# Performance work log

Measured on AMD Instinct MI355X. Metric: run time of the kernel, lower is better.

Reference implementation:

```python
import jax, jax.numpy as jnp
import numpy as np

B, T, D = 16, 2048, 256

def setup_inputs() -> dict:
    key = jax.random.key(0)
    k1, k2, k3 = jax.random.split(key, 3)
    q = jax.random.normal(k1, (B, T, D), dtype=jnp.float32)
    a = jax.random.normal(k2, (B, T, D), dtype=jnp.float32)
    # original uses 'uniform' init; scale ~ small
    U = jax.random.uniform(k3, (D, D), dtype=jnp.float32, minval=-0.05, maxval=0.05)
    return {"q": q, "a": a, "U": U}

def reference(q, a, U):
    # G[b,i,j] = tanh( (q[b,i,:] @ U) . a[b,j,:] )
    qU = jnp.einsum('btd,de->bte', q, U)                 # [B,Tq,D]
    G = jnp.tanh(jnp.einsum('btd,bsd->bts', qU, a))      # [B,Tq,Ta]
    g_q = jax.nn.softmax(jnp.max(G, axis=-1), axis=1)    # [B,Tq]
    g_a = jax.nn.softmax(jnp.max(G, axis=1), axis=1)     # [B,Ta]
    q_out = jnp.einsum('btd,bt->bd', q, g_q)             # [B,D]
    a_out = jnp.einsum('bsd,bs->bd', a, g_a)             # [B,D]
    return (q_out, a_out)
```

## Files before the change

kernel.cpp:

```cpp
#include <hip/hip_runtime.h>
#include <stdint.h>

typedef __attribute__((ext_vector_type(8))) short s8v;
typedef __attribute__((ext_vector_type(4))) float f4v;

__device__ __forceinline__ unsigned short f2bf(float f) {
  unsigned u = __float_as_uint(f);
  u = u + 0x7FFFu + ((u >> 16) & 1u);
  return (unsigned short)(u >> 16);
}
__device__ __forceinline__ unsigned encf(float f) {
  unsigned i = __float_as_uint(f);
  return (i & 0x80000000u) ? ~i : (i | 0x80000000u);
}
__device__ __forceinline__ float decf(unsigned u) {
  unsigned i = (u & 0x80000000u) ? (u & 0x7FFFFFFFu) : ~u;
  return __uint_as_float(i);
}
__device__ __forceinline__ void gload_lds16(const unsigned short* g, unsigned short* l) {
  __builtin_amdgcn_global_load_lds((const __attribute__((address_space(1))) void*)g,
                                   (__attribute__((address_space(3))) void*)l, 16, 0, 0);
}

__global__ void convert_kernel(const float4* __restrict__ q, const float4* __restrict__ a,
                               const float* __restrict__ U,
                               ushort4* __restrict__ qb, ushort4* __restrict__ ab,
                               unsigned short* __restrict__ Ut,
                               unsigned* __restrict__ rcmax, float* __restrict__ out) {
  const int bx = blockIdx.x;
  if (bx < 8192) {
    const int i = bx * 256 + threadIdx.x;
    float4 v = q[i];
    qb[i] = make_ushort4(f2bf(v.x), f2bf(v.y), f2bf(v.z), f2bf(v.w));
    float4 w = a[i];
    ab[i] = make_ushort4(f2bf(w.x), f2bf(w.y), f2bf(w.z), f2bf(w.w));
  } else if (bx < 8256) {
    const int idx = (bx - 8192) * 256 + threadIdx.x;
    const int n  = idx >> 6;
    const int k4 = (idx & 63) * 4;
    ushort4 o;
    o.x = f2bf(U[(k4 + 0) * 256 + n]);
    o.y = f2bf(U[(k4 + 1) * 256 + n]);
    o.z = f2bf(U[(k4 + 2) * 256 + n]);
    o.w = f2bf(U[(k4 + 3) * 256 + n]);
    *(ushort4*)&Ut[n * 256 + k4] = o;
  } else if (bx < 8320) {
    const int idx = (bx - 8256) * 256 + threadIdx.x;
    *(uint4*)&rcmax[idx * 4] = make_uint4(0u, 0u, 0u, 0u);
  } else {
    out[(bx - 8320) * 256 + threadIdx.x] = 0.f;
  }
}

__global__ __attribute__((amdgpu_flat_work_group_size(512, 512), amdgpu_waves_per_eu(2, 2)))
void fused_qu_smax(const unsigned short* __restrict__ qb,
                   const unsigned short* __restrict__ Ut,
                   const unsigned short* __restrict__ ab,
                   unsigned* __restrict__ rowmax,
                   unsigned* __restrict__ colmax) {
  extern __shared__ char smem[];
  unsigned short* qUs    = (unsigned short*)smem;
  unsigned short* Bs2    = (unsigned short*)(smem + 65536);
  unsigned*       colLds = (unsigned*)(smem + 131072);
  unsigned*       rowLds = (unsigned*)(smem + 139264);

  const int tid = threadIdx.x;
  const int b = blockIdx.x, tm = blockIdx.y;

  const int lane = tid & 63;
  const int m16  = lane & 15;
  const int quad = lane >> 4;
  const int wave = tid >> 6;
  const int wm   = wave >> 2;
  const int wn   = wave & 3;
  const int wr32 = (wave >> 1) * 32;
  const int wc64 = (wave & 1) * 64;
  const int srow = tid >> 3;
  const int scol = (((tid & 7) ^ (srow & 7))) * 8;

  #pragma unroll
  for (int i = 0; i < 4; ++i) colLds[i * 512 + tid] = 0u;
  if (tid < 128) rowLds[tid] = 0u;

  const unsigned short* Aq = qb + ((long)b * 2048 + tm * 128) * 256;
  {
    f4v acc[4][4] = {};

#define STAGE1(kt, dst) do {                                                   \
    const int k0_ = (kt) * 64;                                                 \
    _Pragma("unroll")                                                          \
    for (int i_ = 0; i_ < 2; ++i_)                                             \
      gload_lds16(Aq + (long)(i_ * 64 + srow) * 256 + k0_ + scol,              \
                  &(dst)[i_ * 4096 + tid * 8]);                                \
    _Pragma("unroll")                                                          \
    for (int i_ = 0; i_ < 4; ++i_)                                             \
      gload_lds16(Ut + (long)(i_ * 64 + srow) * 256 + k0_ + scol,              \
                  &(dst)[8192 + i_ * 4096 + tid * 8]);                         \
  } while (0)

#define COMPUTE1(buf) do {                                                     \
    _Pragma("unroll")                                                          \
    for (int kk_ = 0; kk_ < 2; ++kk_) {                                        \
      const int cs_ = ((kk_ * 4 + quad) ^ (m16 & 7)) * 8;                      \
      s8v af_[4], bf_[4];                                                      \
      _Pragma("unroll")                                                        \
      for (int i_ = 0; i_ < 4; ++i_)                                           \
        af_[i_] = *(const s8v*)&(buf)[(wm * 64 + i_ * 16 + m16) * 64 + cs_];   \
      _Pragma("unroll")                                                        \
      for (int j_ = 0; j_ < 4; ++j_)                                           \
        bf_[j_] = *(const s8v*)&(buf)[8192 + (wn * 64 + j_ * 16 + m16) * 64 + cs_]; \
      _Pragma("unroll")                                                        \
      for (int i_ = 0; i_ < 4; ++i_)                                           \
        _Pragma("unroll")                                                      \
        for (int j_ = 0; j_ < 4; ++j_)                                         \
          acc[i_][j_] = __builtin_amdgcn_mfma_f32_16x16x32_bf16(af_[i_], bf_[j_], acc[i_][j_], 0, 0, 0); \
    }                                                                          \
  } while (0)

    STAGE1(0, Bs2);
    STAGE1(1, qUs);
    asm volatile("s_waitcnt vmcnt(6)" ::: "memory");
    __builtin_amdgcn_s_barrier();
    COMPUTE1(Bs2);
    __builtin_amdgcn_s_barrier();
    STAGE1(2, Bs2);
    asm volatile("s_waitcnt vmcnt(6)" ::: "memory");
    __builtin_amdgcn_s_barrier();
    COMPUTE1(qUs);
    __builtin_amdgcn_s_barrier();
    STAGE1(3, qUs);
    asm volatile("s_waitcnt vmcnt(6)" ::: "memory");
    __builtin_amdgcn_s_barrier();
    COMPUTE1(Bs2);
    asm volatile("s_waitcnt vmcnt(0)" ::: "memory");
    __builtin_amdgcn_s_barrier();
    COMPUTE1(qUs);
    __syncthreads();

    #pragma unroll
    for (int i = 0; i < 4; ++i)
      #pragma unroll
      for (int r = 0; r < 4; ++r) {
        const int lr = wm * 64 + i * 16 + quad * 4 + r;
        #pragma unroll
        for (int j = 0; j < 4; ++j) {
          const int col = wn * 64 + j * 16 + m16;
          const int ch = (col >> 3) ^ (lr & 7);
          qUs[lr * 256 + ch * 8 + (col & 7)] = f2bf(acc[i][j][r]);
        }
      }
  }
  __syncthreads();

  const unsigned short* Ab_ = ab + (long)b * 2048 * 256;

#define STAGE_TILE(tb, dst) do {                                               \
    _Pragma("unroll")                                                          \
    for (int e_ = 0; e_ < 8; ++e_) {                                           \
      const int u_ = e_ * 512 + tid;                                           \
      const int row_ = u_ >> 5;                                                \
      const int chs_ = (u_ & 31) ^ (row_ & 7);                                 \
      gload_lds16(Ab_ + (long)((tb) * 128 + row_) * 256 + chs_ * 8,            \
                  &(dst)[u_ * 8]);                                             \
    }                                                                          \
  } while (0)

#define COMPUTE_TILE(tb, buf) do {                                             \
    f4v acc[2][4] = {};                                                        \
    _Pragma("unroll")                                                          \
    for (int kq_ = 0; kq_ < 8; ++kq_) {                                        \
      const int cs_ = ((kq_ * 4 + quad) ^ (m16 & 7)) * 8;                      \
      _Pragma("unroll")                                                        \
      for (int j_ = 0; j_ < 4; ++j_) {                                         \
        const s8v bv_ = *(const s8v*)&(buf)[(wc64 + j_ * 16 + m16) * 256 + cs_]; \
        acc[0][j_] = __builtin_amdgcn_mfma_f32_16x16x32_bf16(aq[0][kq_], bv_, acc[0][j_], 0, 0, 0); \
        acc[1][j_] = __builtin_amdgcn_mfma_f32_16x16x32_bf16(aq[1][kq_], bv_, acc[1][j_], 0, 0, 0); \
      }                                                                        \
    }                                                                          \
    _Pragma("unroll")                                                          \
    for (int i_ = 0; i_ < 2; ++i_)                                             \
      _Pragma("unroll")                                                        \
      for (int r_ = 0; r_ < 4; ++r_)                                           \
        rmx[i_][r_] = fmaxf(rmx[i_][r_],                                       \
          fmaxf(fmaxf(acc[i_][0][r_], acc[i_][1][r_]),                         \
                fmaxf(acc[i_][2][r_], acc[i_][3][r_])));                       \
    _Pragma("unroll")                                                          \
    for (int j_ = 0; j_ < 4; ++j_) {                                           \
      float v_ = fmaxf(fmaxf(acc[0][j_][0], acc[0][j_][1]),                    \
                       fmaxf(acc[0][j_][2], acc[0][j_][3]));                   \
      v_ = fmaxf(v_, fmaxf(fmaxf(acc[1][j_][0], acc[1][j_][1]),                \
                           fmaxf(acc[1][j_][2], acc[1][j_][3])));              \
      v_ = fmaxf(v_, __shfl_xor(v_, 16));                                      \
      v_ = fmaxf(v_, __shfl_xor(v_, 32));                                      \
      if (quad == 0)                                                           \
        atomicMax(&colLds[(tb) * 128 + wc64 + j_ * 16 + m16], encf(v_));       \
    }                                                                          \
  } while (0)

  STAGE_TILE(0, Bs2);

  s8v aq[2][8];
  #pragma unroll
  for (int kq = 0; kq < 8; ++kq) {
    const int cs = ((kq * 4 + quad) ^ (m16 & 7)) * 8;
    aq[0][kq] = *(const s8v*)&qUs[(wr32 + m16) * 256 + cs];
    aq[1][kq] = *(const s8v*)&qUs[(wr32 + 16 + m16) * 256 + cs];
  }
  asm volatile("s_waitcnt lgkmcnt(0)" ::: "memory");
  __builtin_amdgcn_s_barrier();

  float rmx[2][4];
  #pragma unroll
  for (int i = 0; i < 2; ++i)
    #pragma unroll
    for (int r = 0; r < 4; ++r) rmx[i][r] = -3.4e38f;

  #pragma unroll 1
  for (int t2 = 0; t2 < 8; ++t2) {
    const int te = t2 * 2;
    STAGE_TILE(te + 1, qUs);
    asm volatile("s_waitcnt vmcnt(8)" ::: "memory");
    __builtin_amdgcn_s_barrier();
    COMPUTE_TILE(te, Bs2);
    __builtin_amdgcn_s_barrier();
    if (te + 2 < 16) {
      STAGE_TILE(te + 2, Bs2);
      asm volatile("s_waitcnt vmcnt(8)" ::: "memory");
    } else {
      asm volatile("s_waitcnt vmcnt(0)" ::: "memory");
    }
    __builtin_amdgcn_s_barrier();
    COMPUTE_TILE(te + 1, qUs);
    __builtin_amdgcn_s_barrier();
  }

  #pragma unroll
  for (int i = 0; i < 2; ++i)
    #pragma unroll
    for (int r = 0; r < 4; ++r) {
      float v = rmx[i][r];
      #pragma unroll
      for (int d2 = 1; d2 < 16; d2 <<= 1) v = fmaxf(v, __shfl_xor(v, d2));
      if (m16 == 0) atomicMax(&rowLds[wr32 + i * 16 + quad * 4 + r], encf(v));
    }
  __syncthreads();
  if (tid < 128)
    rowmax[(long)b * 2048 + tm * 128 + tid] = rowLds[tid];
  #pragma unroll
  for (int i = 0; i < 4; ++i)
    atomicMax(&colmax[(long)b * 2048 + i * 512 + tid], colLds[i * 512 + tid]);
}

__global__ void wsum_kernel(const uint4* __restrict__ qb, const uint4* __restrict__ ab,
                            const unsigned* __restrict__ rowmax, const unsigned* __restrict__ colmax,
                            float* __restrict__ out) {
  const int tid = threadIdx.x;
  const int chunk = blockIdx.x;
  const int b = blockIdx.y;
  const int z = blockIdx.z;
  const unsigned* e = z ? colmax : rowmax;
  const uint4* src = z ? ab : qb;

  __shared__ float sm[4];
  __shared__ float ss[4];
  __shared__ float wLds[128];
  __shared__ float red[256 * 8];

  float x[8];
  float m = -3.4e38f;
  #pragma unroll
  for (int j = 0; j < 8; ++j) {
    x[j] = tanhf(decf(e[b * 2048 + j * 256 + tid]));
    m = fmaxf(m, x[j]);
  }
  #pragma unroll
  for (int d2 = 1; d2 < 64; d2 <<= 1) m = fmaxf(m, __shfl_xor(m, d2));
  if ((tid & 63) == 0) sm[tid >> 6] = m;
  __syncthreads();
  m = fmaxf(fmaxf(sm[0], sm[1]), fmaxf(sm[2], sm[3]));
  float s = 0.f;
  #pragma unroll
  for (int j = 0; j < 8; ++j) s += expf(x[j] - m);
  #pragma unroll
  for (int d2 = 1; d2 < 64; d2 <<= 1) s += __shfl_xor(s, d2);
  if ((tid & 63) == 0) ss[tid >> 6] = s;
  __syncthreads();
  const float inv = 1.f / (ss[0] + ss[1] + ss[2] + ss[3]);

  if (tid < 128) {
    float xv = tanhf(decf(e[b * 2048 + chunk * 128 + tid]));
    wLds[tid] = expf(xv - m) * inv;
  }
  __syncthreads();

  const int dg = tid & 31;
  const int rg = tid >> 5;
  float acc[8] = {};
  const long rowbase = (long)b * 2048 + chunk * 128;
  for (int t = rg; t < 128; t += 8) {
    const float wgt = wLds[t];
    uint4 v = src[(rowbase + t) * 32 + dg];
    acc[0] += wgt * __uint_as_float(v.x << 16);
    acc[1] += wgt * __uint_as_float(v.x & 0xFFFF0000u);
    acc[2] += wgt * __uint_as_float(v.y << 16);
    acc[3] += wgt * __uint_as_float(v.y & 0xFFFF0000u);
    acc[4] += wgt * __uint_as_float(v.z << 16);
    acc[5] += wgt * __uint_as_float(v.z & 0xFFFF0000u);
    acc[6] += wgt * __uint_as_float(v.w << 16);
    acc[7] += wgt * __uint_as_float(v.w & 0xFFFF0000u);
  }
  #pragma unroll
  for (int k = 0; k < 8; ++k) red[tid * 8 + k] = acc[k];
  __syncthreads();
  if (tid < 32) {
    #pragma unroll
    for (int k = 0; k < 8; ++k) {
      float v = 0.f;
      #pragma unroll
      for (int g = 0; g < 8; ++g) v += red[((g << 5) | tid) * 8 + k];
      atomicAdd(&out[z * 4096 + b * 256 + tid * 8 + k], v);
    }
  }
}

extern "C" void kernel_launch(void* const* d_in, const int* in_sizes, int n_in,
                              void* d_out, int out_size, void* d_ws, size_t ws_size,
                              hipStream_t stream) {
  const float* q = (const float*)d_in[0];
  const float* a = (const float*)d_in[1];
  const float* U = (const float*)d_in[2];
  float* out = (float*)d_out;

  char* w = (char*)d_ws;
  unsigned short* qb = (unsigned short*)w;
  unsigned short* ab = (unsigned short*)(w + (16ull << 20));
  unsigned short* Ut = (unsigned short*)(w + (32ull << 20));
  unsigned* rmax = (unsigned*)(w + (32ull << 20) + (128ull << 10));
  unsigned* cmax = rmax + 32768;

  constexpr int SMEM = 139776;
  hipFuncSetAttribute((const void*)fused_qu_smax,
                      hipFuncAttributeMaxDynamicSharedMemorySize, SMEM);

  convert_kernel<<<8352, 256, 0, stream>>>((const float4*)q, (const float4*)a, U,
                                           (ushort4*)qb, (ushort4*)ab, Ut, rmax, out);

  fused_qu_smax<<<dim3(16, 16), 512, SMEM, stream>>>(qb, Ut, ab, rmax, cmax);

  wsum_kernel<<<dim3(16, 16, 2), 256, 0, stream>>>((const uint4*)qb, (const uint4*)ab,
                                                   rmax, cmax, out);
}
```

Measured before the change: 157.4 us.

## Restructure a-tile loop into 4-buffer 64-row pipeline with prefetch during qU phase

Replaces the double-buffered 128-row a-tile loop with a four-slot ring of 64-row tiles, three tiles in flight, so global loads overlap more MFMA work. The first a tiles are issued during the tail of the qU GEMM phase, and a full __syncthreads is replaced by an lgkmcnt wait plus barrier. The smaller tiles halve the MFMA work per barrier and double the number of barriers and colmax atomics. The reused LDS regions depend on correct wait counts.

```diff
diff --git a/kernel.cpp b/kernel.cpp
--- a/kernel.cpp
+++ b/kernel.cpp
@@ -63,6 +63,7 @@
   unsigned short* Bs2    = (unsigned short*)(smem + 65536);
   unsigned*       colLds = (unsigned*)(smem + 131072);
   unsigned*       rowLds = (unsigned*)(smem + 139264);
+#define SBUF(k) ((unsigned short*)(smem + ((k) << 15)))
 
   const int tid = threadIdx.x;
   const int b = blockIdx.x, tm = blockIdx.y;
@@ -74,13 +75,26 @@
   const int wm   = wave >> 2;
   const int wn   = wave & 3;
   const int wr32 = (wave >> 1) * 32;
-  const int wc64 = (wave & 1) * 64;
+  const int wc32 = (wave & 1) * 32;
   const int srow = tid >> 3;
   const int scol = (((tid & 7) ^ (srow & 7))) * 8;
 
   #pragma unroll
   for (int i = 0; i < 4; ++i) colLds[i * 512 + tid] = 0u;
   if (tid < 128) rowLds[tid] = 0u;
+
+  const unsigned short* Ab_ = ab + (long)b * 2048 * 256;
+
+#define STG64(tb, dst) do {                                                    \
+    _Pragma("unroll")                                                          \
+    for (int e_ = 0; e_ < 4; ++e_) {                                           \
+      const int u_ = e_ * 512 + tid;         \
+      const int row_ = u_ >> 5;                                                \
+      const int chs_ = (u_ & 31) ^ (row_ & 7);                                 \
+      gload_lds16(Ab_ + (long)((tb) * 64 + row_) * 256 + chs_ * 8,             \
+                  &(dst)[u_ * 8]);                                             \
+    }                                                                          \
+  } while (0)
 
   const unsigned short* Aq = qb + ((long)b * 2048 + tm * 128) * 256;
   {
@@ -134,8 +148,11 @@
     COMPUTE1(Bs2);
     asm volatile("s_waitcnt vmcnt(0)" ::: "memory");
     __builtin_amdgcn_s_barrier();
+    STG64(0, SBUF(2));
+    STG64(1, SBUF(3));
     COMPUTE1(qUs);
-    __syncthreads();
+    asm volatile("s_waitcnt lgkmcnt(0)" ::: "memory");
+    __builtin_amdgcn_s_barrier();
 
     #pragma unroll
     for (int i = 0; i < 4; ++i)
@@ -150,29 +167,34 @@
         }
       }
   }
-  __syncthreads();
-
-  const unsigned short* Ab_ = ab + (long)b * 2048 * 256;
-
-#define STAGE_TILE(tb, dst) do {                                               \
-    _Pragma("unroll")                                                          \
-    for (int e_ = 0; e_ < 8; ++e_) {                                           \
-      const int u_ = e_ * 512 + tid;                                           \
-      const int row_ = u_ >> 5;                                                \
-      const int chs_ = (u_ & 31) ^ (row_ & 7);                                 \
-      gload_lds16(Ab_ + (long)((tb) * 128 + row_) * 256 + chs_ * 8,            \
-                  &(dst)[u_ * 8]);                                             \
-    }                                                                          \
-  } while (0)
-
-#define COMPUTE_TILE(tb, buf) do {                                             \
-    f4v acc[2][4] = {};                                                        \
+  asm volatile("s_waitcnt lgkmcnt(0)" ::: "memory");
+  __builtin_amdgcn_s_barrier();
+
+  s8v aq[2][8];
+  #pragma unroll
+  for (int kq = 0; kq < 8; ++kq) {
+    const int cs = ((kq * 4 + quad) ^ (m16 & 7)) * 8;
+    aq[0][kq] = *(const s8v*)&qUs[(wr32 + m16) * 256 + cs];
+    aq[1][kq] = *(const s8v*)&qUs[(wr32 + 16 + m16) * 256 + cs];
+  }
+  asm volatile("s_waitcnt lgkmcnt(0)" ::: "memory");
+  __builtin_amdgcn_s_barrier();
+  STG64(2, SBUF(0));
+
+  float rmx[2][4];
+  #pragma unroll
+  for (int i = 0; i < 2; ++i)
+    #pragma unroll
+    for (int r = 0; r < 4; ++r) rmx[i][r] = -3.4e38f;
+
+#define CMP64(tb, buf) do {                                                    \
+    f4v acc[2][2] = {};                                                        \
     _Pragma("unroll")                                                          \
     for (int kq_ = 0; kq_ < 8; ++kq_) {                                        \
       const int cs_ = ((kq_ * 4 + quad) ^ (m16 & 7)) * 8;                      \
       _Pragma("unroll")                                                        \
-      for (int j_ = 0; j_ < 4; ++j_) {                                         \
-        const s8v bv_ = *(const s8v*)&(buf)[(wc64 + j_ * 16 + m16) * 256 + cs_]; \
+      for (int j_ = 0; j_ < 2; ++j_) {                                         \
+        const s8v bv_ = *(const s8v*)&(buf)[(wc32 + j_ * 16 + m16) * 256 + cs_]; \
         acc[0][j_] = __builtin_amdgcn_mfma_f32_16x16x32_bf16(aq[0][kq_], bv_, acc[0][j_], 0, 0, 0); \
         acc[1][j_] = __builtin_amdgcn_mfma_f32_16x16x32_bf16(aq[1][kq_], bv_, acc[1][j_], 0, 0, 0); \
       }                                                                        \
@@ -181,11 +203,9 @@
     for (int i_ = 0; i_ < 2; ++i_)                                             \
       _Pragma("unroll")                                                        \
       for (int r_ = 0; r_ < 4; ++r_)                                           \
-        rmx[i_][r_] = fmaxf(rmx[i_][r_],                                       \
-          fmaxf(fmaxf(acc[i_][0][r_], acc[i_][1][r_]),                         \
-                fmaxf(acc[i_][2][r_], acc[i_][3][r_])));                       \
-    _Pragma("unroll")                                                          \
-    for (int j_ = 0; j_ < 4; ++j_) {                                           \
+        rmx[i_][r_] = fmaxf(rmx[i_][r_], fmaxf(acc[i_][0][r_], acc[i_][1][r_])); \
+    _Pragma("unroll")                                                          \
+    for (int j_ = 0; j_ < 2; ++j_) {                                           \
       float v_ = fmaxf(fmaxf(acc[0][j_][0], acc[0][j_][1]),                    \
                        fmaxf(acc[0][j_][2], acc[0][j_][3]));                   \
       v_ = fmaxf(v_, fmaxf(fmaxf(acc[1][j_][0], acc[1][j_][1]),                \
@@ -193,46 +213,25 @@
       v_ = fmaxf(v_, __shfl_xor(v_, 16));                                      \
       v_ = fmaxf(v_, __shfl_xor(v_, 32));                                      \
       if (quad == 0)                                                           \
-        atomicMax(&colLds[(tb) * 128 + wc64 + j_ * 16 + m16], encf(v_));       \
+        atomicMax(&colLds[(tb) * 64 + wc32 + j_ * 16 + m16], encf(v_));        \
     }                                                                          \
   } while (0)
 
-  STAGE_TILE(0, Bs2);
-
-  s8v aq[2][8];
-  #pragma unroll
-  for (int kq = 0; kq < 8; ++kq) {
-    const int cs = ((kq * 4 + quad) ^ (m16 & 7)) * 8;
-    aq[0][kq] = *(const s8v*)&qUs[(wr32 + m16) * 256 + cs];
-    aq[1][kq] = *(const s8v*)&qUs[(wr32 + 16 + m16) * 256 + cs];
-  }
-  asm volatile("s_waitcnt lgkmcnt(0)" ::: "memory");
-  __builtin_amdgcn_s_barrier();
-
-  float rmx[2][4];
-  #pragma unroll
-  for (int i = 0; i < 2; ++i)
-    #pragma unroll
-    for (int r = 0; r < 4; ++r) rmx[i][r] = -3.4e38f;
-
   #pragma unroll 1
-  for (int t2 = 0; t2 < 8; ++t2) {
-    const int te = t2 * 2;
-    STAGE_TILE(te + 1, qUs);
+  for (int t = 0; t < 30; ++t) {
     asm volatile("s_waitcnt vmcnt(8)" ::: "memory");
     __builtin_amdgcn_s_barrier();
-    COMPUTE_TILE(te, Bs2);
-    __builtin_amdgcn_s_barrier();
-    if (te + 2 < 16) {
-      STAGE_TILE(te + 2, Bs2);
-      asm volatile("s_waitcnt vmcnt(8)" ::: "memory");
-    } else {
-      asm volatile("s_waitcnt vmcnt(0)" ::: "memory");
-    }
-    __builtin_amdgcn_s_barrier();
-    COMPUTE_TILE(te + 1, qUs);
-    __builtin_amdgcn_s_barrier();
-  }
+    if (t <= 28) STG64(t + 3, SBUF((t + 1) & 3));
+    CMP64(t, SBUF((t + 2) & 3));
+    __builtin_amdgcn_s_barrier();
+  }
+  asm volatile("s_waitcnt vmcnt(4)" ::: "memory");
+  __builtin_amdgcn_s_barrier();
+  CMP64(30, SBUF(0));
+  __builtin_amdgcn_s_barrier();
+  asm volatile("s_waitcnt vmcnt(0)" ::: "memory");
+  __builtin_amdgcn_s_barrier();
+  CMP64(31, SBUF(1));
 
   #pragma unroll
   for (int i = 0; i < 2; ++i)
```

Measured after the change: 156.4 us. Within noise of the previous version (-0.6%).
